# Performance work log

Measured on AMD Instinct MI355X. Metric: run time of the kernel, lower is better.

## Reference

```python
import jax, jax.numpy as jnp
import numpy as np

N, K, DIM = 50000, 16, 256
SLOPE = 0.2

def _leaky(x):
    return jnp.where(x >= 0, x, SLOPE * x)

def _mlp(x, w, b):
    # torch nn.Linear followed by LeakyReLU(0.2); w is [in, out]
    return _leaky(x @ w + b)

def setup_inputs() -> dict:
    key = jax.random.key(0)
    ks = jax.random.split(key, 14)
    d4, d2 = DIM // 4, DIM // 2
    def lin(k, i, o):
        kw, kb = jax.random.split(k)
        s = 1.0 / np.sqrt(i)
        return (jax.random.uniform(kw, (i, o), jnp.float32, -s, s),
                jax.random.uniform(kb, (o,), jnp.float32, -s, s))
    w_res, b_res = lin(ks[0], DIM, DIM)
    w_init, b_init = lin(ks[1], DIM, d4)
    w_g1, b_g1 = lin(ks[2], 4, d4)
    w_g2, b_g2 = lin(ks[3], 4, d2)
    w_fin, b_fin = lin(ks[4], DIM, DIM)
    return {
        "input_features": jax.random.normal(ks[5], (N, DIM), jnp.float32),
        "geom_features": jax.random.normal(ks[6], (N, K, 4), jnp.float32),
        "closest_indices": jax.random.randint(ks[7], (N, K), 0, N, jnp.int32),
        "w_res": w_res, "b_res": b_res,
        "w_init": w_init, "b_init": b_init,
        "w_g1": w_g1, "b_g1": b_g1,
        "w_g2": w_g2, "b_g2": b_g2,
        "w_fin": w_fin, "b_fin": b_fin,
    }

def _lfa(feat, geom, idx, w_g, b_g):
    # feat: [N, d]; geom: [N, K, 4]; idx: [N, K]
    g = _mlp(geom, w_g, b_g)                 # [N, K, d]
    gathered = feat[idx]                      # [N, K, d] gather over points
    combined = jnp.concatenate([g, gathered], axis=-1)  # [N, K, 2d]
    return jnp.mean(combined, axis=1)         # [N, 2d]

def reference(input_features, geom_features, closest_indices,
              w_res, b_res, w_init, b_init, w_g1, b_g1, w_g2, b_g2,
              w_fin, b_fin):
    residual = _mlp(input_features, w_res, b_res)            # [N, DIM]
    a = _mlp(input_features, w_init, b_init)                 # [N, DIM/4]
    a = _lfa(a, geom_features, closest_indices, w_g1, b_g1)  # [N, DIM/2]
    a = _lfa(a, geom_features, closest_indices, w_g2, b_g2)  # [N, DIM]
    a = _mlp(a, w_fin, b_fin)                                # [N, DIM]
    return a + residual
```

## Files before the change

### kernel.cpp

```cpp
#include <hip/hip_runtime.h>

#define DIM 256
#define KNN 16
#define SLOPE 0.2f

typedef unsigned short u16;
typedef __attribute__((ext_vector_type(8))) unsigned short u16x8;
typedef __attribute__((ext_vector_type(4))) unsigned short u16x4;
typedef __attribute__((ext_vector_type(8))) short s16x8;
typedef __attribute__((ext_vector_type(4))) float f32x4;

__device__ __forceinline__ float leaky(float x) { return x >= 0.f ? x : SLOPE * x; }
__device__ __forceinline__ u16 f2bu(float f) {
    unsigned int u = __float_as_uint(f);
    u = (u + 0x7FFFu + ((u >> 16) & 1u)) >> 16;
    return (u16)u;
}
__device__ __forceinline__ float bu2f(u16 h) {
    return __uint_as_float(((unsigned int)h) << 16);
}

__global__ __launch_bounds__(256) void k_prep(
    const float* __restrict__ w_res, const float* __restrict__ w_init,
    const float* __restrict__ w_fin, u16* __restrict__ wT1, u16* __restrict__ wT3)
{
    const int c = blockIdx.x, t = threadIdx.x;
    if (c < 256)      wT1[c * 256 + t] = f2bu(w_res[t * 256 + c]);
    else if (c < 320) wT1[c * 256 + t] = f2bu(w_init[t * 64 + (c - 256)]);
    else              wT3[(c - 320) * 256 + t] = f2bu(w_fin[t * 256 + (c - 320)]);
}

#define APAD 264
#define BPAD 40
__global__ __launch_bounds__(256) void k_gemm1(
    const float* __restrict__ in, const u16* __restrict__ wT1,
    const float* __restrict__ b_res, const float* __restrict__ b_init,
    float* __restrict__ resid, u16* __restrict__ a1, int N)
{
    __shared__ u16 A_s[64 * APAD];
    __shared__ u16 B_s[320 * BPAD];
    const int t = threadIdx.x;
    const int base = blockIdx.x * 64;

    {
        const int row = t >> 2, seg = t & 3;
        const int grow = min(base + row, N - 1);
        const float* src = in + (size_t)grow * DIM + seg * 64;
        u16* dst = &A_s[row * APAD + seg * 64];
        #pragma unroll
        for (int j = 0; j < 8; ++j) {
            float4 f0 = *(const float4*)(src + j * 8);
            float4 f1 = *(const float4*)(src + j * 8 + 4);
            u16x8 p;
            p[0] = f2bu(f0.x); p[1] = f2bu(f0.y); p[2] = f2bu(f0.z); p[3] = f2bu(f0.w);
            p[4] = f2bu(f1.x); p[5] = f2bu(f1.y); p[6] = f2bu(f1.z); p[7] = f2bu(f1.w);
            *(u16x8*)(dst + j * 8) = p;
        }
    }

    f32x4 acc[4][5];
    #pragma unroll
    for (int i = 0; i < 4; ++i)
        #pragma unroll
        for (int j = 0; j < 5; ++j)
            acc[i][j] = (f32x4){0.f, 0.f, 0.f, 0.f};

    const int w = t >> 6, lane = t & 63;
    const int llow = lane & 15, lhi = lane >> 4;

    for (int ks = 0; ks < 8; ++ks) {
        u16x8 breg[5];
        #pragma unroll
        for (int j = 0; j < 5; ++j) {
            int id = t + 256 * j;
            int col = id >> 2, kg = id & 3;
            breg[j] = *(const u16x8*)(wT1 + col * 256 + ks * 32 + kg * 8);
        }
        __syncthreads();
        #pragma unroll
        for (int j = 0; j < 5; ++j) {
            int id = t + 256 * j;
            int col = id >> 2, kg = id & 3;
            *(u16x8*)(&B_s[col * BPAD + kg * 8]) = breg[j];
        }
        __syncthreads();

        s16x8 afrag[4];
        #pragma unroll
        for (int rt = 0; rt < 4; ++rt)
            afrag[rt] = *(const s16x8*)(&A_s[(rt * 16 + llow) * APAD + ks * 32 + lhi * 8]);
        #pragma unroll
        for (int ci = 0; ci < 5; ++ci) {
            const int ct = w * 5 + ci;
            s16x8 bfrag = *(const s16x8*)(&B_s[(ct * 16 + llow) * BPAD + lhi * 8]);
            #pragma unroll
            for (int rt = 0; rt < 4; ++rt)
                acc[rt][ci] = __builtin_amdgcn_mfma_f32_16x16x32_bf16(
                    afrag[rt], bfrag, acc[rt][ci], 0, 0, 0);
        }
    }

    #pragma unroll
    for (int ci = 0; ci < 5; ++ci) {
        const int ct = w * 5 + ci;
        const int col = ct * 16 + llow;
        if (col < 256) {
            const float bias = b_res[col];
            #pragma unroll
            for (int rt = 0; rt < 4; ++rt)
                #pragma unroll
                for (int r = 0; r < 4; ++r) {
                    int row = base + rt * 16 + lhi * 4 + r;
                    if (row < N)
                        resid[(size_t)row * DIM + col] = leaky(acc[rt][ci][r] + bias);
                }
        } else {
            const int c2 = col - 256;
            const float bias = b_init[c2];
            #pragma unroll
            for (int rt = 0; rt < 4; ++rt)
                #pragma unroll
                for (int r = 0; r < 4; ++r) {
                    int row = base + rt * 16 + lhi * 4 + r;
                    if (row < N)
                        a1[(size_t)row * 64 + c2] = f2bu(leaky(acc[rt][ci][r] + bias));
                }
        }
    }
}

__global__ __launch_bounds__(256) void k_lfa1(
    const float* __restrict__ geom, const int* __restrict__ idx,
    const float* __restrict__ w_g1, const float* __restrict__ b_g1,
    const u16* __restrict__ a1, u16* __restrict__ a2, int N)
{
    __shared__ float geom_s[16 * KNN * 4];
    __shared__ int idx_s[16 * KNN];
    const int t = threadIdx.x;
    const int base = blockIdx.x * 16;

    {
        size_t off = (size_t)base * 64 + t * 4;
        size_t mx = (size_t)N * 64 - 4;
        if (off > mx) off = mx;
        *(float4*)&geom_s[t * 4] = *(const float4*)(geom + off);
        idx_s[t] = idx[min(base * KNN + t, N * KNN - 1)];
    }
    __syncthreads();

    const int pt = t >> 4, s = t & 15;
    const int n = base + pt;

    float wr[4][4], bb[4];
    #pragma unroll
    for (int r = 0; r < 4; ++r)
        #pragma unroll
        for (int j = 0; j < 4; ++j)
            wr[r][j] = w_g1[r * 64 + s * 4 + j];
    #pragma unroll
    for (int j = 0; j < 4; ++j) bb[j] = b_g1[s * 4 + j];

    float accM[4] = {0.f, 0.f, 0.f, 0.f};
    const float4* g4 = (const float4*)&geom_s[pt * 64];
    #pragma unroll
    for (int k = 0; k < KNN; ++k) {
        float4 g = g4[k];
        #pragma unroll
        for (int j = 0; j < 4; ++j)
            accM[j] += leaky(g.x * wr[0][j] + g.y * wr[1][j] + g.z * wr[2][j] + g.w * wr[3][j] + bb[j]);
    }

    float accG[4] = {0.f, 0.f, 0.f, 0.f};
    u16x4 v[KNN];
    #pragma unroll
    for (int k = 0; k < KNN; ++k)
        v[k] = *(const u16x4*)(a1 + (size_t)idx_s[pt * KNN + k] * 64 + s * 4);
    #pragma unroll
    for (int k = 0; k < KNN; ++k)
        #pragma unroll
        for (int j = 0; j < 4; ++j) accG[j] += bu2f(v[k][j]);

    if (n < N) {
        u16x4 pm, pg;
        #pragma unroll
        for (int j = 0; j < 4; ++j) {
            pm[j] = f2bu(accM[j] * 0.0625f);
            pg[j] = f2bu(accG[j] * 0.0625f);
        }
        *(u16x4*)(a2 + (size_t)n * 128 + s * 4) = pm;
        *(u16x4*)(a2 + (size_t)n * 128 + 64 + s * 4) = pg;
    }
}

__global__ __launch_bounds__(256) void k_gather3(
    const int* __restrict__ idx, const u16* __restrict__ a2,
    u16* __restrict__ a3h, int N)
{
    __shared__ int idx_s[16 * KNN];
    const int t = threadIdx.x;
    const int base = blockIdx.x * 16;
    idx_s[t] = idx[min(base * KNN + t, N * KNN - 1)];
    __syncthreads();

    const int pt = t >> 4, s = t & 15;
    const int n = base + pt;

    u16x8 v[KNN];
    #pragma unroll
    for (int k = 0; k < KNN; ++k)
        v[k] = *(const u16x8*)(a2 + (size_t)idx_s[pt * KNN + k] * 128 + s * 8);

    float acc[8] = {0.f, 0.f, 0.f, 0.f, 0.f, 0.f, 0.f, 0.f};
    #pragma unroll
    for (int k = 0; k < KNN; ++k)
        #pragma unroll
        for (int j = 0; j < 8; ++j) acc[j] += bu2f(v[k][j]);

    u16x8 p;
    #pragma unroll
    for (int j = 0; j < 8; ++j) p[j] = f2bu(acc[j] * 0.0625f);
    if (n < N) *(u16x8*)(a3h + (size_t)n * 128 + s * 8) = p;
}

__global__ __launch_bounds__(256) void k_gemm3(
    const float* __restrict__ geom, const float* __restrict__ w_g2,
    const float* __restrict__ b_g2, const u16* __restrict__ a3h,
    const u16* __restrict__ wT3, const float* __restrict__ b_fin,
    float* __restrict__ out, int N)
{
    __shared__ u16 A_s[64 * APAD];
    __shared__ u16 B_s[256 * BPAD];
    __shared__ float geom_s[64 * 64];
    const int t = threadIdx.x;
    const int base = blockIdx.x * 64;

    {
        size_t mx = (size_t)N * 64 - 4;
        #pragma unroll
        for (int j = 0; j < 4; ++j) {
            size_t off = (size_t)base * 64 + t * 4 + j * 1024;
            if (off > mx) off = mx;
            *(float4*)&geom_s[t * 4 + j * 1024] = *(const float4*)(geom + off);
        }
        const int row = t >> 2, q = t & 3;
        const int grow = min(base + row, N - 1);
        const u16* src = a3h + (size_t)grow * 128 + q * 32;
        u16* dst = &A_s[row * APAD + 128 + q * 32];
        #pragma unroll
        for (int j = 0; j < 4; ++j)
            *(u16x8*)(dst + j * 8) = *(const u16x8*)(src + j * 8);
    }
    __syncthreads();

    {
        const int c = t & 127, h = t >> 7;
        const float w0 = w_g2[c], w1 = w_g2[128 + c], w2 = w_g2[256 + c],
                    w3 = w_g2[384 + c], bb = b_g2[c];
        #pragma unroll 4
        for (int p = 0; p < 32; ++p) {
            const int pt = h * 32 + p;
            const float4* g4 = (const float4*)&geom_s[pt * 64];
            float acc = 0.f;
            #pragma unroll
            for (int k = 0; k < KNN; ++k) {
                float4 g = g4[k];
                acc += leaky(g.x * w0 + g.y * w1 + g.z * w2 + g.w * w3 + bb);
            }
            A_s[pt * APAD + c] = f2bu(acc * 0.0625f);
        }
    }

    f32x4 acc[4][4];
    #pragma unroll
    for (int i = 0; i < 4; ++i)
        #pragma unroll
        for (int j = 0; j < 4; ++j)
            acc[i][j] = (f32x4){0.f, 0.f, 0.f, 0.f};

    const int w = t >> 6, lane = t & 63;
    const int llow = lane & 15, lhi = lane >> 4;

    for (int ks = 0; ks < 8; ++ks) {
        u16x8 breg[4];
        #pragma unroll
        for (int kg = 0; kg < 4; ++kg)
            breg[kg] = *(const u16x8*)(wT3 + t * 256 + ks * 32 + kg * 8);
        __syncthreads();
        #pragma unroll
        for (int kg = 0; kg < 4; ++kg)
            *(u16x8*)(&B_s[t * BPAD + kg * 8]) = breg[kg];
        __syncthreads();

        s16x8 afrag[4];
        #pragma unroll
        for (int rt = 0; rt < 4; ++rt)
            afrag[rt] = *(const s16x8*)(&A_s[(rt * 16 + llow) * APAD + ks * 32 + lhi * 8]);
        #pragma unroll
        for (int ci = 0; ci < 4; ++ci) {
            const int ct = w * 4 + ci;
            s16x8 bfrag = *(const s16x8*)(&B_s[(ct * 16 + llow) * BPAD + lhi * 8]);
            #pragma unroll
            for (int rt = 0; rt < 4; ++rt)
                acc[rt][ci] = __builtin_amdgcn_mfma_f32_16x16x32_bf16(
                    afrag[rt], bfrag, acc[rt][ci], 0, 0, 0);
        }
    }

    #pragma unroll
    for (int ci = 0; ci < 4; ++ci) {
        const int ct = w * 4 + ci;
        const int col = ct * 16 + llow;
        const float bias = b_fin[col];
        #pragma unroll
        for (int rt = 0; rt < 4; ++rt)
            #pragma unroll
            for (int r = 0; r < 4; ++r) {
                int row = base + rt * 16 + lhi * 4 + r;
                if (row < N) {
                    size_t o = (size_t)row * DIM + col;
                    out[o] = leaky(acc[rt][ci][r] + bias) + out[o];
                }
            }
    }
}

extern "C" void kernel_launch(void* const* d_in, const int* in_sizes, int n_in,
                              void* d_out, int out_size, void* d_ws, size_t ws_size,
                              hipStream_t stream) {
    const float* in    = (const float*)d_in[0];
    const float* geom  = (const float*)d_in[1];
    const int*   idx   = (const int*)d_in[2];
    const float* w_res = (const float*)d_in[3];
    const float* b_res = (const float*)d_in[4];
    const float* w_init= (const float*)d_in[5];
    const float* b_init= (const float*)d_in[6];
    const float* w_g1  = (const float*)d_in[7];
    const float* b_g1  = (const float*)d_in[8];
    const float* w_g2  = (const float*)d_in[9];
    const float* b_g2  = (const float*)d_in[10];
    const float* w_fin = (const float*)d_in[11];
    const float* b_fin = (const float*)d_in[12];
    float* out = (float*)d_out;

    const int N = in_sizes[0] / DIM;

    char* ws = (char*)d_ws;
    u16* a1  = (u16*)ws;
    u16* a3h = (u16*)ws;
    u16* a2  = (u16*)(ws + (size_t)N * 128 * 2);
    u16* wT1 = (u16*)(ws + (size_t)N * 256 * 2);
    u16* wT3 = wT1 + 320 * 256;

    k_prep<<<576, 256, 0, stream>>>(w_res, w_init, w_fin, wT1, wT3);
    k_gemm1<<<(N + 63) / 64, 256, 0, stream>>>(in, wT1, b_res, b_init, out, a1, N);
    k_lfa1<<<(N + 15) / 16, 256, 0, stream>>>(geom, idx, w_g1, b_g1, a1, a2, N);
    k_gather3<<<(N + 15) / 16, 256, 0, stream>>>(idx, a2, a3h, N);
    k_gemm3<<<(N + 63) / 64, 256, 0, stream>>>(geom, w_g2, b_g2, a3h, wT3, b_fin, out, N);
}
```

Measured before the change: 310.3 us.

## Split geometry MLP out of final GEMM into separate kernel

Moves the second LFA geometry MLP (per-point mean of leaky(geom·w_g2+b)) out of the final GEMM kernel into a new kernel that writes bf16 results to the workspace, reusing the a2 buffer. The GEMM kernel now just loads both halves of its A tile from global memory. It also drops the large geometry shared-memory buffer and adds a minimum-blocks-per-SM hint of 3, aiming for more occupancy and better latency hiding in the GEMM. The cost is an extra launch plus an extra global write and read of an N×128 bf16 intermediate.

```diff
diff --git a/kernel.cpp b/kernel.cpp
--- a/kernel.cpp
+++ b/kernel.cpp
@@ -222,52 +222,71 @@
     if (n < N) *(u16x8*)(a3h + (size_t)n * 128 + s * 8) = p;
 }
 
-__global__ __launch_bounds__(256) void k_gemm3(
+__global__ __launch_bounds__(256) void k_mlp3(
     const float* __restrict__ geom, const float* __restrict__ w_g2,
-    const float* __restrict__ b_g2, const u16* __restrict__ a3h,
+    const float* __restrict__ b_g2, u16* __restrict__ a3m, int N)
+{
+    __shared__ float geom_s[16 * 64];
+    const int t = threadIdx.x;
+    const int base = blockIdx.x * 16;
+    {
+        size_t off = (size_t)base * 64 + t * 4;
+        size_t mx = (size_t)N * 64 - 4;
+        if (off > mx) off = mx;
+        *(float4*)&geom_s[t * 4] = *(const float4*)(geom + off);
+    }
+    __syncthreads();
+
+    const int pt = t >> 4, s = t & 15;
+    const int n = base + pt;
+
+    float w0[8], w1[8], w2[8], w3[8], bb[8];
+    #pragma unroll
+    for (int j = 0; j < 8; ++j) {
+        w0[j] = w_g2[s * 8 + j];
+        w1[j] = w_g2[128 + s * 8 + j];
+        w2[j] = w_g2[256 + s * 8 + j];
+        w3[j] = w_g2[384 + s * 8 + j];
+        bb[j] = b_g2[s * 8 + j];
+    }
+
+    float acc[8] = {0.f, 0.f, 0.f, 0.f, 0.f, 0.f, 0.f, 0.f};
+    const float4* g4 = (const float4*)&geom_s[pt * 64];
+    #pragma unroll
+    for (int k = 0; k < KNN; ++k) {
+        float4 g = g4[k];
+        #pragma unroll
+        for (int j = 0; j < 8; ++j)
+            acc[j] += leaky(g.x * w0[j] + g.y * w1[j] + g.z * w2[j] + g.w * w3[j] + bb[j]);
+    }
+
+    if (n < N) {
+        u16x8 p;
+        #pragma unroll
+        for (int j = 0; j < 8; ++j) p[j] = f2bu(acc[j] * 0.0625f);
+        *(u16x8*)(a3m + (size_t)n * 128 + s * 8) = p;
+    }
+}
+
+__global__ __launch_bounds__(256, 3) void k_gemm3(
+    const u16* __restrict__ a3m, const u16* __restrict__ a3h,
     const u16* __restrict__ wT3, const float* __restrict__ b_fin,
     float* __restrict__ out, int N)
 {
     __shared__ u16 A_s[64 * APAD];
     __shared__ u16 B_s[256 * BPAD];
-    __shared__ float geom_s[64 * 64];
     const int t = threadIdx.x;
     const int base = blockIdx.x * 64;
 
     {
-        size_t mx = (size_t)N * 64 - 4;
-        #pragma unroll
-        for (int j = 0; j < 4; ++j) {
-            size_t off = (size_t)base * 64 + t * 4 + j * 1024;
-            if (off > mx) off = mx;
-            *(float4*)&geom_s[t * 4 + j * 1024] = *(const float4*)(geom + off);
-        }
         const int row = t >> 2, q = t & 3;
         const int grow = min(base + row, N - 1);
-        const u16* src = a3h + (size_t)grow * 128 + q * 32;
-        u16* dst = &A_s[row * APAD + 128 + q * 32];
-        #pragma unroll
-        for (int j = 0; j < 4; ++j)
+        const u16* src = (q < 2) ? (a3m + (size_t)grow * 128 + q * 64)
+                                 : (a3h + (size_t)grow * 128 + (q - 2) * 64);
+        u16* dst = &A_s[row * APAD + q * 64];
+        #pragma unroll
+        for (int j = 0; j < 8; ++j)
             *(u16x8*)(dst + j * 8) = *(const u16x8*)(src + j * 8);
-    }
-    __syncthreads();
-
-    {
-        const int c = t & 127, h = t >> 7;
-        const float w0 = w_g2[c], w1 = w_g2[128 + c], w2 = w_g2[256 + c],
-                    w3 = w_g2[384 + c], bb = b_g2[c];
-        #pragma unroll 4
-        for (int p = 0; p < 32; ++p) {
-            const int pt = h * 32 + p;
-            const float4* g4 = (const float4*)&geom_s[pt * 64];
-            float acc = 0.f;
-            #pragma unroll
-            for (int k = 0; k < KNN; ++k) {
-                float4 g = g4[k];
-                acc += leaky(g.x * w0 + g.y * w1 + g.z * w2 + g.w * w3 + bb);
-            }
-            A_s[pt * APAD + c] = f2bu(acc * 0.0625f);
-        }
     }
 
     f32x4 acc[4][4];
@@ -348,6 +367,7 @@
     u16* a1  = (u16*)ws;
     u16* a3h = (u16*)ws;
     u16* a2  = (u16*)(ws + (size_t)N * 128 * 2);
+    u16* a3m = a2;
     u16* wT1 = (u16*)(ws + (size_t)N * 256 * 2);
     u16* wT3 = wT1 + 320 * 256;
 
@@ -355,5 +375,6 @@
     k_gemm1<<<(N + 63) / 64, 256, 0, stream>>>(in, wT1, b_res, b_init, out, a1, N);
     k_lfa1<<<(N + 15) / 16, 256, 0, stream>>>(geom, idx, w_g1, b_g1, a1, a2, N);
     k_gather3<<<(N + 15) / 16, 256, 0, stream>>>(idx, a2, a3h, N);
-    k_gemm3<<<(N + 63) / 64, 256, 0, stream>>>(geom, w_g2, b_g2, a3h, wT3, b_fin, out, N);
-}
+    k_mlp3<<<(N + 15) / 16, 256, 0, stream>>>(geom, w_g2, b_g2, a3m, N);
+    k_gemm3<<<(N + 63) / 64, 256, 0, stream>>>(a3m, a3h, wT3, b_fin, out, N);
+}
```

Result: faster. 296.7 us (-4.4%).
